# Performance work log

Measured on AMD Instinct MI355X. Metric: run time of the kernel, lower is better.

The kernel has to match this reference:

```python
import jax, jax.numpy as jnp
import numpy as np

N = 30000      # nodes
E = 1000000    # edges
G = 256        # graphs
IN = 3         # in_channels
H = 8          # heads
D = 16         # per-head dim
HID = 128      # hidden_dim = H*D
L = 3          # num_layers
KP = 17        # num_keypoints
KPE = 16       # kp_emb_dim
NEG = 0.2      # GATv2 leaky_relu negative slope
EPS = 1e-5     # BatchNorm eps


def setup_inputs() -> dict:
    key = jax.random.key(0)
    ks = jax.random.split(key, 24)
    x = jax.random.normal(ks[0], (N, IN), jnp.float32)
    edge_index = jax.random.randint(ks[1], (2, E), 0, N, jnp.int32)
    batch = jnp.sort(jax.random.randint(ks[2], (N,), 0, G, jnp.int32))
    s_in = 1.0 / np.sqrt(IN + KPE)
    s_h = 1.0 / np.sqrt(HID)
    return {
        "x": x,
        "edge_index": edge_index,
        "batch": batch,
        "kp_emb": jax.random.normal(ks[3], (KP, KPE), jnp.float32),
        "w_in": jax.random.normal(ks[4], (IN + KPE, HID), jnp.float32) * s_in,
        "b_in": jax.random.normal(ks[5], (HID,), jnp.float32) * 0.01,
        "w_l": jax.random.normal(ks[6], (L, HID, HID), jnp.float32) * s_h,
        "w_r": jax.random.normal(ks[7], (L, HID, HID), jnp.float32) * s_h,
        "att": jax.random.normal(ks[8], (L, H, D), jnp.float32) * (1.0 / np.sqrt(D)),
        "conv_bias": jax.random.normal(ks[9], (L, HID), jnp.float32) * 0.01,
        "bn_gamma": jnp.ones((L, HID), jnp.float32) + 0.1 * jax.random.normal(ks[10], (L, HID), jnp.float32),
        "bn_beta": 0.1 * jax.random.normal(ks[11], (L, HID), jnp.float32),
        "bn_mean": 0.1 * jax.random.normal(ks[12], (L, HID), jnp.float32),
        "bn_var": 0.5 + jax.random.uniform(ks[13], (L, HID), jnp.float32),
        "w1": jax.random.normal(ks[14], (HID, 2 * HID), jnp.float32) * s_h,
        "b1": jnp.zeros((2 * HID,), jnp.float32),
        "w2": jax.random.normal(ks[15], (2 * HID, HID), jnp.float32) * (1.0 / np.sqrt(2 * HID)),
        "b2": jnp.zeros((HID,), jnp.float32),
        "w3": jax.random.normal(ks[16], (HID, 2), jnp.float32) * s_h,
        "b3": jnp.zeros((2,), jnp.float32),
    }


def reference(x, edge_index, batch, kp_emb, w_in, b_in, w_l, w_r, att, conv_bias,
              bn_gamma, bn_beta, bn_mean, bn_var, w1, b1, w2, b2, w3, b3):
    n = x.shape[0]
    # keypoint id embedding concat + input projection
    kp_ids = jnp.arange(n) % KP
    h = jnp.concatenate([x, kp_emb[kp_ids]], axis=-1) @ w_in + b_in  # [N, HID]
    # GATv2Conv adds self loops by default
    loops = jnp.arange(n, dtype=edge_index.dtype)
    src = jnp.concatenate([edge_index[0], loops])  # message sources (j)
    dst = jnp.concatenate([edge_index[1], loops])  # message targets (i)
    for l in range(L):
        xl = (h @ w_l[l]).reshape(n, H, D)  # source transform (lin_l)
        xr = (h @ w_r[l]).reshape(n, H, D)  # target transform (lin_r)
        z = xl[src] + xr[dst]                              # [Et, H, D]
        score = jnp.einsum('ehd,hd->eh', jax.nn.leaky_relu(z, NEG), att[l])
        # segment softmax over incoming edges of each dst node
        m = jax.ops.segment_max(score, dst, num_segments=n)
        ex = jnp.exp(score - m[dst])
        denom = jax.ops.segment_sum(ex, dst, num_segments=n)
        alpha = ex / denom[dst]                            # [Et, H]
        msg = xl[src] * alpha[..., None]                   # [Et, H, D]
        out = jax.ops.segment_sum(msg, dst, num_segments=n).reshape(n, HID) + conv_bias[l]
        out = jax.nn.relu(out)
        # BatchNorm1d (eval mode: running stats)
        out = (out - bn_mean[l]) * (bn_gamma[l] / jnp.sqrt(bn_var[l] + EPS)) + bn_beta[l]
        h = h + out  # residual (dropout = identity in eval)
    # global mean pool per graph
    sums = jax.ops.segment_sum(h, batch, num_segments=G)
    cnt = jax.ops.segment_sum(jnp.ones((n, 1), h.dtype), batch, num_segments=G)
    g = sums / jnp.maximum(cnt, 1.0)
    # classifier MLP
    g = jax.nn.elu(g @ w1 + b1)
    g = jax.nn.elu(g @ w2 + b2)
    return g @ w3 + b3  # [G, 2]
```

## Files before the change

kernel.cpp:

```cpp
#include <hip/hip_runtime.h>
#include <hip/hip_bf16.h>

#define N_NODES 30000
#define N_EDGES 1000000
#define N_GRAPHS 256
#define HEADS 8
#define DHEAD 16
#define HIDDEN 128
#define LAYERS 3
#define KPN 17
#define KPE 16
#define NEG_SLOPE 0.2f
#define BN_EPS 1e-5f
#define ET (N_EDGES + N_NODES)
#define NBIN 235
#define BINW 128
#define BINCAP 6144
#define CHUNK 4096

typedef __attribute__((ext_vector_type(8))) short bf16x8;
typedef __attribute__((ext_vector_type(4))) float f32x4;

__device__ __forceinline__ unsigned bf16_rne(float f) {
    unsigned u = __float_as_uint(f);
    return (u + 0x7fffu + ((u >> 16) & 1u)) >> 16;
}

__global__ __launch_bounds__(256) void k_bin(const int* __restrict__ ei,
                                             int* __restrict__ bcnt,
                                             unsigned* __restrict__ bdata) {
    __shared__ int lcnt[NBIN];
    __shared__ int lbase[NBIN];
    int base = blockIdx.x * CHUNK;
    int n = N_EDGES - base; if (n > CHUNK) n = CHUNK;
    for (int i = threadIdx.x; i < NBIN; i += 256) lcnt[i] = 0;
    __syncthreads();
    for (int t = threadIdx.x; t < n; t += 256) {
        int d = ei[N_EDGES + base + t];
        atomicAdd(&lcnt[d >> 7], 1);
    }
    __syncthreads();
    for (int i = threadIdx.x; i < NBIN; i += 256) {
        int c = lcnt[i];
        lbase[i] = c ? atomicAdd(&bcnt[i], c) : 0;
        lcnt[i] = 0;
    }
    __syncthreads();
    for (int t = threadIdx.x; t < n; t += 256) {
        int s = ei[base + t];
        int d = ei[N_EDGES + base + t];
        int b = d >> 7;
        int pos = lbase[b] + atomicAdd(&lcnt[b], 1);
        bdata[(size_t)b * BINCAP + pos] = (unsigned)s | ((unsigned)(d & 127) << 15);
    }
}

__global__ __launch_bounds__(256) void k_aux(const int* __restrict__ bcnt,
                                             const int* __restrict__ batch,
                                             const float* __restrict__ w_l,
                                             const float* __restrict__ w_r,
                                             int* __restrict__ bbase,
                                             int* __restrict__ ptr,
                                             int* __restrict__ gptr,
                                             unsigned short* __restrict__ wT) {
    int t = threadIdx.x;
    if (blockIdx.x == 0) {
        for (int g = t; g <= N_GRAPHS; g += 256) {
            if (g == N_GRAPHS) { gptr[g] = N_NODES; }
            else {
                int lo = 0, hi = N_NODES;
                while (lo < hi) {
                    int mid = (lo + hi) >> 1;
                    if (batch[mid] < g) lo = mid + 1; else hi = mid;
                }
                gptr[g] = lo;
            }
        }
        __shared__ int v[256];
        int c = 0;
        if (t < NBIN) {
            int nodes = N_NODES - t * BINW; if (nodes > BINW) nodes = BINW;
            c = bcnt[t] + nodes;
        }
        v[t] = c;
        __syncthreads();
        for (int off = 1; off < 256; off <<= 1) {
            int x = (t >= off) ? v[t - off] : 0;
            __syncthreads();
            v[t] += x;
            __syncthreads();
        }
        if (t < NBIN) bbase[t] = v[t] - c;
        if (t == 0) ptr[N_NODES] = ET;
    } else {
        int idx = (blockIdx.x - 1) * 256 + t;
        if (idx < LAYERS * 256 * 128) {
            int l = idx / (256 * 128);
            int rem = idx - l * 256 * 128;
            int c = rem >> 7;
            int k = rem & 127;
            float v = (c < 128) ? w_l[(size_t)l * 16384 + k * 128 + c]
                                : w_r[(size_t)l * 16384 + k * 128 + (c - 128)];
            wT[idx] = (unsigned short)bf16_rne(v);
        }
    }
}

__global__ __launch_bounds__(256) void k_place2(const int* __restrict__ bcnt,
                                                const unsigned* __restrict__ bdata,
                                                const int* __restrict__ bbase,
                                                int* __restrict__ ptr,
                                                unsigned short* __restrict__ csr_src) {
    __shared__ int hist[BINW];
    __shared__ int pre[BINW];
    __shared__ int nodestart[BINW];
    __shared__ int lofs[BINW];
    int b = blockIdx.x;
    int tid = threadIdx.x;
    int nNodes = N_NODES - b * BINW; if (nNodes > BINW) nNodes = BINW;
    int n = bcnt[b];
    if (tid < BINW) hist[tid] = (tid < nNodes) ? 1 : 0;
    __syncthreads();
    for (int t = tid; t < n; t += 256)
        atomicAdd(&hist[(bdata[(size_t)b * BINCAP + t] >> 15) & 127], 1);
    __syncthreads();
    if (tid < BINW) pre[tid] = hist[tid];
    __syncthreads();
    for (int off = 1; off < BINW; off <<= 1) {
        int x = (tid >= off && tid < BINW) ? pre[tid - off] : 0;
        __syncthreads();
        if (tid < BINW) pre[tid] += x;
        __syncthreads();
    }
    if (tid < BINW) {
        int ns = bbase[b] + pre[tid] - hist[tid];
        nodestart[tid] = ns;
        if (tid < nNodes) {
            int node = b * BINW + tid;
            ptr[node] = ns;
            csr_src[ns] = (unsigned short)node;
        }
        lofs[tid] = 1;
    }
    __syncthreads();
    for (int t = tid; t < n; t += 256) {
        unsigned e = bdata[(size_t)b * BINCAP + t];
        int dl = (e >> 15) & 127;
        int pos = nodestart[dl] + atomicAdd(&lofs[dl], 1);
        csr_src[pos] = (unsigned short)(e & 0x7fffu);
    }
}

__global__ void k_inproj(const float* __restrict__ x, const float* __restrict__ kp_emb,
                         const float* __restrict__ w_in, const float* __restrict__ b_in,
                         float* __restrict__ h, unsigned short* __restrict__ hb) {
    int t = blockIdx.x * 256 + threadIdx.x;
    if (t >= N_NODES * HIDDEN) return;
    int c = t & 127, i = t >> 7;
    float acc = b_in[c];
    const float* xi = x + i * 3;
    acc += xi[0] * w_in[0 * 128 + c];
    acc += xi[1] * w_in[1 * 128 + c];
    acc += xi[2] * w_in[2 * 128 + c];
    const float* kp = kp_emb + (i % KPN) * KPE;
#pragma unroll
    for (int k = 0; k < KPE; ++k) acc += kp[k] * w_in[(3 + k) * 128 + c];
    h[t] = acc;
    hb[t] = (unsigned short)bf16_rne(acc);
}

__global__ __launch_bounds__(256) void k_gemm(const unsigned short* __restrict__ hb,
                                              const unsigned short* __restrict__ wT,
                                              unsigned short* __restrict__ xlb,
                                              unsigned short* __restrict__ xrb) {
    int wave = threadIdx.x >> 6;
    int lane = threadIdx.x & 63;
    int brow = blockIdx.x * 32;
    int lr = lane & 15;
    int lk = lane >> 4;
    int ar0 = brow + lr;
    int ar1 = brow + 16 + lr;
    int ar0c = ar0 < N_NODES ? ar0 : N_NODES - 1;
    int ar1c = ar1 < N_NODES ? ar1 : N_NODES - 1;
    int c0 = wave * 64 + lr;

    const unsigned short* ha0 = hb + (size_t)ar0c * 128 + lk * 8;
    const unsigned short* ha1 = hb + (size_t)ar1c * 128 + lk * 8;
    const unsigned short* wb  = wT + (size_t)c0 * 128 + lk * 8;

    f32x4 acc[2][4];
#pragma unroll
    for (int m = 0; m < 2; ++m)
#pragma unroll
        for (int n = 0; n < 4; ++n) acc[m][n] = (f32x4){0.f, 0.f, 0.f, 0.f};

#pragma unroll
    for (int ks = 0; ks < 4; ++ks) {
        bf16x8 a0 = *(const bf16x8*)(ha0 + ks * 32);
        bf16x8 a1 = *(const bf16x8*)(ha1 + ks * 32);
#pragma unroll
        for (int nt = 0; nt < 4; ++nt) {
            bf16x8 b = *(const bf16x8*)(wb + nt * 16 * 128 + ks * 32);
            acc[0][nt] = __builtin_amdgcn_mfma_f32_16x16x32_bf16(a0, b, acc[0][nt], 0, 0, 0);
            acc[1][nt] = __builtin_amdgcn_mfma_f32_16x16x32_bf16(a1, b, acc[1][nt], 0, 0, 0);
        }
    }

    int drow0 = brow + lk * 4;
#pragma unroll
    for (int mt = 0; mt < 2; ++mt) {
#pragma unroll
        for (int nt = 0; nt < 4; ++nt) {
            int col = c0 + nt * 16;
#pragma unroll
            for (int j = 0; j < 4; ++j) {
                int grow = drow0 + mt * 16 + j;
                if (grow >= N_NODES) continue;
                unsigned short bv = (unsigned short)bf16_rne(acc[mt][nt][j]);
                if (col < 128) xlb[(size_t)grow * 128 + col] = bv;
                else           xrb[(size_t)grow * 128 + (col - 128)] = bv;
            }
        }
    }
}

__global__ __launch_bounds__(256) void k_gat(const uint4* __restrict__ xlb4,
                                             const uint4* __restrict__ xrb4,
                                             const int* __restrict__ ptr,
                                             const unsigned short* __restrict__ csr_src,
                                             const float* __restrict__ att_l,
                                             const float* __restrict__ bias_l,
                                             const float* __restrict__ gamma_l,
                                             const float* __restrict__ beta_l,
                                             const float* __restrict__ mean_l,
                                             const float* __restrict__ var_l,
                                             float* __restrict__ h,
                                             unsigned short* __restrict__ hb) {
    int wid = (blockIdx.x * 256 + threadIdx.x) >> 6;
    int lane = threadIdx.x & 63;
    if (wid >= N_NODES) return;
    int i = wid;
    int e4 = lane >> 4;
    int l16 = lane & 15;
    int d0 = 8 * l16;

    uint4 xw = xrb4[(size_t)i * 16 + l16];
    float2 xra = make_float2(__uint_as_float(xw.x << 16), __uint_as_float(xw.x & 0xffff0000u));
    float2 xrb_ = make_float2(__uint_as_float(xw.y << 16), __uint_as_float(xw.y & 0xffff0000u));
    float2 xrc = make_float2(__uint_as_float(xw.z << 16), __uint_as_float(xw.z & 0xffff0000u));
    float2 xrd = make_float2(__uint_as_float(xw.w << 16), __uint_as_float(xw.w & 0xffff0000u));
    const float L2E = 1.44269504089f;
    float4 avA = *(const float4*)(att_l + d0);
    float4 avB = *(const float4*)(att_l + d0 + 4);
    float2 a6a = make_float2(avA.x * (0.6f * L2E), avA.y * (0.6f * L2E));
    float2 a6b = make_float2(avA.z * (0.6f * L2E), avA.w * (0.6f * L2E));
    float2 a6c = make_float2(avB.x * (0.6f * L2E), avB.y * (0.6f * L2E));
    float2 a6d = make_float2(avB.z * (0.6f * L2E), avB.w * (0.6f * L2E));
    float2 a4a = make_float2(avA.x * (0.4f * L2E), avA.y * (0.4f * L2E));
    float2 a4b = make_float2(avA.z * (0.4f * L2E), avA.w * (0.4f * L2E));
    float2 a4c = make_float2(avB.x * (0.4f * L2E), avB.y * (0.4f * L2E));
    float2 a4d = make_float2(avB.z * (0.4f * L2E), avB.w * (0.4f * L2E));
    int e0 = ptr[i], e1 = ptr[i + 1];

    float denom = 0.f;
    float2 acA = make_float2(0.f, 0.f), acB = make_float2(0.f, 0.f);
    float2 acC = make_float2(0.f, 0.f), acD = make_float2(0.f, 0.f);

#define LDQ(KQ, WREG, VREG) { \
    int eo = 4 * (KQ) + e4; \
    int sr = __shfl(sv, eo); \
    VREG = eo < cnt; \
    int rw = VREG ? sr : 0; \
    WREG = xlb4[(size_t)rw * 16 + l16]; \
}
#define PROCQ(WREG, VREG) { \
    float2 va = make_float2(__uint_as_float(WREG.x << 16), __uint_as_float(WREG.x & 0xffff0000u)); \
    float2 vb = make_float2(__uint_as_float(WREG.y << 16), __uint_as_float(WREG.y & 0xffff0000u)); \
    float2 vc = make_float2(__uint_as_float(WREG.z << 16), __uint_as_float(WREG.z & 0xffff0000u)); \
    float2 vd = make_float2(__uint_as_float(WREG.w << 16), __uint_as_float(WREG.w & 0xffff0000u)); \
    float2 za, zb, zc, zd; \
    za.x = va.x + xra.x;  za.y = va.y + xra.y; \
    zb.x = vb.x + xrb_.x; zb.y = vb.y + xrb_.y; \
    zc.x = vc.x + xrc.x;  zc.y = vc.y + xrc.y; \
    zd.x = vd.x + xrd.x;  zd.y = vd.y + xrd.y; \
    float2 p6, p4; \
    p6.x = za.x * a6a.x;  p6.y = za.y * a6a.y; \
    p6.x = fmaf(zb.x, a6b.x, p6.x); p6.y = fmaf(zb.y, a6b.y, p6.y); \
    p6.x = fmaf(zc.x, a6c.x, p6.x); p6.y = fmaf(zc.y, a6c.y, p6.y); \
    p6.x = fmaf(zd.x, a6d.x, p6.x); p6.y = fmaf(zd.y, a6d.y, p6.y); \
    p4.x = fabsf(za.x) * a4a.x;  p4.y = fabsf(za.y) * a4a.y; \
    p4.x = fmaf(fabsf(zb.x), a4b.x, p4.x); p4.y = fmaf(fabsf(zb.y), a4b.y, p4.y); \
    p4.x = fmaf(fabsf(zc.x), a4c.x, p4.x); p4.y = fmaf(fabsf(zc.y), a4c.y, p4.y); \
    p4.x = fmaf(fabsf(zd.x), a4d.x, p4.x); p4.y = fmaf(fabsf(zd.y), a4d.y, p4.y); \
    float p = (p6.x + p4.x) + (p6.y + p4.y); \
    p += __shfl_xor(p, 1); \
    float ex = VREG ? exp2f(p) : 0.f; \
    denom += ex; \
    acA.x = fmaf(ex, va.x, acA.x); acA.y = fmaf(ex, va.y, acA.y); \
    acB.x = fmaf(ex, vb.x, acB.x); acB.y = fmaf(ex, vb.y, acB.y); \
    acC.x = fmaf(ex, vc.x, acC.x); acC.y = fmaf(ex, vc.y, acC.y); \
    acD.x = fmaf(ex, vd.x, acD.x); acD.y = fmaf(ex, vd.y, acD.y); \
}

    for (int base = e0; base < e1; base += 64) {
        int idx = base + lane;
        int sv = (idx < e1) ? (int)csr_src[idx] : 0;
        int cnt = e1 - base; if (cnt > 64) cnt = 64;
        int nq = (cnt + 3) >> 2;

        uint4 w0, w1; bool b0 = false, b1 = false;
        LDQ(0, w0, b0);
        if (1 < nq) LDQ(1, w1, b1);
        int k = 0;
        for (; k + 2 < nq; k += 2) {
            uint4 n0, n1; bool c0v, c1v;
            LDQ(k + 2, n0, c0v);
            LDQ(k + 3, n1, c1v);
            PROCQ(w0, b0); PROCQ(w1, b1);
            w0 = n0; b0 = c0v; w1 = n1; b1 = c1v;
        }
        PROCQ(w0, b0);
        if (k + 1 < nq) PROCQ(w1, b1);
    }
#undef LDQ
#undef PROCQ

    denom += __shfl_xor(denom, 16); denom += __shfl_xor(denom, 32);
    acA.x += __shfl_xor(acA.x, 16); acA.x += __shfl_xor(acA.x, 32);
    acA.y += __shfl_xor(acA.y, 16); acA.y += __shfl_xor(acA.y, 32);
    acB.x += __shfl_xor(acB.x, 16); acB.x += __shfl_xor(acB.x, 32);
    acB.y += __shfl_xor(acB.y, 16); acB.y += __shfl_xor(acB.y, 32);
    acC.x += __shfl_xor(acC.x, 16); acC.x += __shfl_xor(acC.x, 32);
    acC.y += __shfl_xor(acC.y, 16); acC.y += __shfl_xor(acC.y, 32);
    acD.x += __shfl_xor(acD.x, 16); acD.x += __shfl_xor(acD.x, 32);
    acD.y += __shfl_xor(acD.y, 16); acD.y += __shfl_xor(acD.y, 32);

    if (e4 == 0) {
        float inv = 1.f / denom;
        float4 biaA = *(const float4*)(bias_l + d0),  biaB = *(const float4*)(bias_l + d0 + 4);
        float4 gamA = *(const float4*)(gamma_l + d0), gamB = *(const float4*)(gamma_l + d0 + 4);
        float4 betA = *(const float4*)(beta_l + d0),  betB = *(const float4*)(beta_l + d0 + 4);
        float4 meaA = *(const float4*)(mean_l + d0),  meaB = *(const float4*)(mean_l + d0 + 4);
        float4 varA = *(const float4*)(var_l + d0),   varB = *(const float4*)(var_l + d0 + 4);
        float o0 = fmaxf(acA.x * inv + biaA.x, 0.f);
        float o1 = fmaxf(acA.y * inv + biaA.y, 0.f);
        float o2 = fmaxf(acB.x * inv + biaA.z, 0.f);
        float o3 = fmaxf(acB.y * inv + biaA.w, 0.f);
        float o4 = fmaxf(acC.x * inv + biaB.x, 0.f);
        float o5 = fmaxf(acC.y * inv + biaB.y, 0.f);
        float o6 = fmaxf(acD.x * inv + biaB.z, 0.f);
        float o7 = fmaxf(acD.y * inv + biaB.w, 0.f);
        o0 = (o0 - meaA.x) * (gamA.x * rsqrtf(varA.x + BN_EPS)) + betA.x;
        o1 = (o1 - meaA.y) * (gamA.y * rsqrtf(varA.y + BN_EPS)) + betA.y;
        o2 = (o2 - meaA.z) * (gamA.z * rsqrtf(varA.z + BN_EPS)) + betA.z;
        o3 = (o3 - meaA.w) * (gamA.w * rsqrtf(varA.w + BN_EPS)) + betA.w;
        o4 = (o4 - meaB.x) * (gamB.x * rsqrtf(varB.x + BN_EPS)) + betB.x;
        o5 = (o5 - meaB.y) * (gamB.y * rsqrtf(varB.y + BN_EPS)) + betB.y;
        o6 = (o6 - meaB.z) * (gamB.z * rsqrtf(varB.z + BN_EPS)) + betB.z;
        o7 = (o7 - meaB.w) * (gamB.w * rsqrtf(varB.w + BN_EPS)) + betB.w;
        float4 hvA = *(const float4*)(h + (size_t)i * 128 + d0);
        float4 hvB = *(const float4*)(h + (size_t)i * 128 + d0 + 4);
        hvA.x += o0; hvA.y += o1; hvA.z += o2; hvA.w += o3;
        hvB.x += o4; hvB.y += o5; hvB.z += o6; hvB.w += o7;
        *(float4*)(h + (size_t)i * 128 + d0) = hvA;
        *(float4*)(h + (size_t)i * 128 + d0 + 4) = hvB;
        uint4 pk;
        pk.x = bf16_rne(hvA.x) | (bf16_rne(hvA.y) << 16);
        pk.y = bf16_rne(hvA.z) | (bf16_rne(hvA.w) << 16);
        pk.z = bf16_rne(hvB.x) | (bf16_rne(hvB.y) << 16);
        pk.w = bf16_rne(hvB.z) | (bf16_rne(hvB.w) << 16);
        *(uint4*)(hb + (size_t)i * 128 + d0) = pk;
    }
}

__global__ __launch_bounds__(256) void k_poolmlp(const float* __restrict__ h,
                                                 const int* __restrict__ gptr,
                                                 const float* __restrict__ w1, const float* __restrict__ b1,
                                                 const float* __restrict__ w2, const float* __restrict__ b2,
                                                 const float* __restrict__ w3, const float* __restrict__ b3,
                                                 float* __restrict__ out) {
    __shared__ float red[256];
    __shared__ float g[128], t1[256], t2[128];
    int b = blockIdx.x, t = threadIdx.x;
    int c = t & 127, half = t >> 7;
    int lo = gptr[b], hi = gptr[b + 1];
    float s = 0.f;
    for (int i = lo + half; i < hi; i += 2) s += h[(size_t)i * 128 + c];
    red[t] = s;
    __syncthreads();
    if (half == 0) {
        float cntf = fmaxf((float)(hi - lo), 1.0f);
        g[c] = (red[c] + red[c + 128]) / cntf;
    }
    __syncthreads();
    {
        float acc = b1[t];
        for (int k = 0; k < 128; ++k) acc += g[k] * w1[k * 256 + t];
        t1[t] = acc > 0.f ? acc : expm1f(acc);
    }
    __syncthreads();
    if (t < 128) {
        float acc = b2[t];
        for (int k = 0; k < 256; ++k) acc += t1[k] * w2[k * 128 + t];
        t2[t] = acc > 0.f ? acc : expm1f(acc);
    }
    __syncthreads();
    if (t < 2) {
        float acc = b3[t];
        for (int k = 0; k < 128; ++k) acc += t2[k] * w3[k * 2 + t];
        out[b * 2 + t] = acc;
    }
}

extern "C" void kernel_launch(void* const* d_in, const int* in_sizes, int n_in,
                              void* d_out, int out_size, void* d_ws, size_t ws_size,
                              hipStream_t stream) {
    const float* x        = (const float*)d_in[0];
    const int*   ei       = (const int*)d_in[1];
    const int*   batch    = (const int*)d_in[2];
    const float* kp_emb   = (const float*)d_in[3];
    const float* w_in     = (const float*)d_in[4];
    const float* b_in     = (const float*)d_in[5];
    const float* w_l      = (const float*)d_in[6];
    const float* w_r      = (const float*)d_in[7];
    const float* att      = (const float*)d_in[8];
    const float* conv_b   = (const float*)d_in[9];
    const float* bn_gamma = (const float*)d_in[10];
    const float* bn_beta  = (const float*)d_in[11];
    const float* bn_mean  = (const float*)d_in[12];
    const float* bn_var   = (const float*)d_in[13];
    const float* w1 = (const float*)d_in[14];
    const float* b1 = (const float*)d_in[15];
    const float* w2 = (const float*)d_in[16];
    const float* b2 = (const float*)d_in[17];
    const float* w3 = (const float*)d_in[18];
    const float* b3 = (const float*)d_in[19];
    float* out = (float*)d_out;

    char* ws = (char*)d_ws;
    const size_t OFF_H    = 0;
    const size_t OFF_HB   = OFF_H    + 15360000;
    const size_t OFF_XL   = OFF_HB   + 7680000;
    const size_t OFF_XR   = OFF_XL   + 7680000;
    const size_t OFF_WT   = OFF_XR   + 7680000;
    const size_t OFF_PTR  = OFF_WT   + 196608;
    const size_t OFF_BCNT = OFF_PTR  + 120320;
    const size_t OFF_BBAS = OFF_BCNT + 1024;
    const size_t OFF_SRC  = OFF_BBAS + 1024;
    const size_t OFF_GPTR = OFF_SRC  + 2060032;

    float*          h      = (float*)(ws + OFF_H);
    unsigned short* hb     = (unsigned short*)(ws + OFF_HB);
    unsigned short* xlb    = (unsigned short*)(ws + OFF_XL);
    unsigned short* xrb    = (unsigned short*)(ws + OFF_XR);
    unsigned*       bdata  = (unsigned*)(ws + OFF_XR);
    unsigned short* wT     = (unsigned short*)(ws + OFF_WT);
    int*            ptr    = (int*)(ws + OFF_PTR);
    int*            bcnt   = (int*)(ws + OFF_BCNT);
    int*            bbase  = (int*)(ws + OFF_BBAS);
    unsigned short* csrsrc = (unsigned short*)(ws + OFF_SRC);
    int*            gptr   = (int*)(ws + OFF_GPTR);

    hipMemsetAsync(bcnt, 0, NBIN * 4, stream);
    k_bin<<<(N_EDGES + CHUNK - 1) / CHUNK, 256, 0, stream>>>(ei, bcnt, bdata);
    k_aux<<<1 + (LAYERS * 256 * 128 + 255) / 256, 256, 0, stream>>>(bcnt, batch, w_l, w_r,
                                                                    bbase, ptr, gptr, wT);
    k_place2<<<NBIN, 256, 0, stream>>>(bcnt, bdata, bbase, ptr, csrsrc);

    k_inproj<<<(N_NODES * 128 + 255) / 256, 256, 0, stream>>>(x, kp_emb, w_in, b_in, h, hb);

    for (int l = 0; l < LAYERS; ++l) {
        k_gemm<<<(N_NODES + 31) / 32, 256, 0, stream>>>(hb, wT + (size_t)l * 256 * 128, xlb, xrb);
        k_gat<<<(N_NODES + 3) / 4, 256, 0, stream>>>(
            (const uint4*)xlb, (const uint4*)xrb, ptr, csrsrc,
            att + (size_t)l * 128, conv_b + (size_t)l * 128,
            bn_gamma + (size_t)l * 128, bn_beta + (size_t)l * 128,
            bn_mean + (size_t)l * 128, bn_var + (size_t)l * 128, h, hb);
    }

    k_poolmlp<<<N_GRAPHS, 256, 0, stream>>>(h, gptr, w1, b1, w2, b2, w3, b3, out);
}
```

Before: 280.3 us.

## Fuse preprocessing kernels, fold input projection into first GEMM, stage GEMM stores

```diff
diff --git a/kernel.cpp b/kernel.cpp
--- a/kernel.cpp
+++ b/kernel.cpp
@@ -17,6 +17,8 @@
 #define BINW 128
 #define BINCAP 6144
 #define CHUNK 4096
+#define NB_EDGE 245
+#define NB_WCONV 384
 
 typedef __attribute__((ext_vector_type(8))) short bf16x8;
 typedef __attribute__((ext_vector_type(4))) float f32x4;
@@ -28,44 +30,40 @@
 
 __global__ __launch_bounds__(256) void k_bin(const int* __restrict__ ei,
                                              int* __restrict__ bcnt,
-                                             unsigned* __restrict__ bdata) {
-    __shared__ int lcnt[NBIN];
-    __shared__ int lbase[NBIN];
-    int base = blockIdx.x * CHUNK;
-    int n = N_EDGES - base; if (n > CHUNK) n = CHUNK;
-    for (int i = threadIdx.x; i < NBIN; i += 256) lcnt[i] = 0;
-    __syncthreads();
-    for (int t = threadIdx.x; t < n; t += 256) {
-        int d = ei[N_EDGES + base + t];
-        atomicAdd(&lcnt[d >> 7], 1);
-    }
-    __syncthreads();
-    for (int i = threadIdx.x; i < NBIN; i += 256) {
-        int c = lcnt[i];
-        lbase[i] = c ? atomicAdd(&bcnt[i], c) : 0;
-        lcnt[i] = 0;
-    }
-    __syncthreads();
-    for (int t = threadIdx.x; t < n; t += 256) {
-        int s = ei[base + t];
-        int d = ei[N_EDGES + base + t];
-        int b = d >> 7;
-        int pos = lbase[b] + atomicAdd(&lcnt[b], 1);
-        bdata[(size_t)b * BINCAP + pos] = (unsigned)s | ((unsigned)(d & 127) << 15);
-    }
-}
-
-__global__ __launch_bounds__(256) void k_aux(const int* __restrict__ bcnt,
+                                             unsigned* __restrict__ bdata,
                                              const int* __restrict__ batch,
+                                             int* __restrict__ gptr,
                                              const float* __restrict__ w_l,
                                              const float* __restrict__ w_r,
-                                             int* __restrict__ bbase,
-                                             int* __restrict__ ptr,
-                                             int* __restrict__ gptr,
                                              unsigned short* __restrict__ wT) {
-    int t = threadIdx.x;
-    if (blockIdx.x == 0) {
-        for (int g = t; g <= N_GRAPHS; g += 256) {
+    int bid = blockIdx.x;
+    if (bid < NB_EDGE) {
+        __shared__ int lcnt[NBIN];
+        __shared__ int lbase[NBIN];
+        int base = bid * CHUNK;
+        int n = N_EDGES - base; if (n > CHUNK) n = CHUNK;
+        for (int i = threadIdx.x; i < NBIN; i += 256) lcnt[i] = 0;
+        __syncthreads();
+        for (int t = threadIdx.x; t < n; t += 256) {
+            int d = ei[N_EDGES + base + t];
+            atomicAdd(&lcnt[d >> 7], 1);
+        }
+        __syncthreads();
+        for (int i = threadIdx.x; i < NBIN; i += 256) {
+            int c = lcnt[i];
+            lbase[i] = c ? atomicAdd(&bcnt[i], c) : 0;
+            lcnt[i] = 0;
+        }
+        __syncthreads();
+        for (int t = threadIdx.x; t < n; t += 256) {
+            int s = ei[base + t];
+            int d = ei[N_EDGES + base + t];
+            int b = d >> 7;
+            int pos = lbase[b] + atomicAdd(&lcnt[b], 1);
+            bdata[(size_t)b * BINCAP + pos] = (unsigned)s | ((unsigned)(d & 127) << 15);
+        }
+    } else if (bid == NB_EDGE) {
+        for (int g = threadIdx.x; g <= N_GRAPHS; g += 256) {
             if (g == N_GRAPHS) { gptr[g] = N_NODES; }
             else {
                 int lo = 0, hi = N_NODES;
@@ -76,24 +74,8 @@
                 gptr[g] = lo;
             }
         }
-        __shared__ int v[256];
-        int c = 0;
-        if (t < NBIN) {
-            int nodes = N_NODES - t * BINW; if (nodes > BINW) nodes = BINW;
-            c = bcnt[t] + nodes;
-        }
-        v[t] = c;
-        __syncthreads();
-        for (int off = 1; off < 256; off <<= 1) {
-            int x = (t >= off) ? v[t - off] : 0;
-            __syncthreads();
-            v[t] += x;
-            __syncthreads();
-        }
-        if (t < NBIN) bbase[t] = v[t] - c;
-        if (t == 0) ptr[N_NODES] = ET;
     } else {
-        int idx = (blockIdx.x - 1) * 256 + t;
+        int idx = (bid - NB_EDGE - 1) * 256 + threadIdx.x;
         if (idx < LAYERS * 256 * 128) {
             int l = idx / (256 * 128);
             int rem = idx - l * 256 * 128;
@@ -104,6 +86,28 @@
             wT[idx] = (unsigned short)bf16_rne(v);
         }
     }
+}
+
+__global__ __launch_bounds__(256) void k_bscan(const int* __restrict__ bcnt,
+                                               int* __restrict__ bbase,
+                                               int* __restrict__ ptr) {
+    __shared__ int v[256];
+    int t = threadIdx.x;
+    int c = 0;
+    if (t < NBIN) {
+        int nodes = N_NODES - t * BINW; if (nodes > BINW) nodes = BINW;
+        c = bcnt[t] + nodes;
+    }
+    v[t] = c;
+    __syncthreads();
+    for (int off = 1; off < 256; off <<= 1) {
+        int x = (t >= off) ? v[t - off] : 0;
+        __syncthreads();
+        v[t] += x;
+        __syncthreads();
+    }
+    if (t < NBIN) bbase[t] = v[t] - c;
+    if (t == 0) ptr[N_NODES] = ET;
 }
 
 __global__ __launch_bounds__(256) void k_place2(const int* __restrict__ bcnt,
@@ -151,42 +155,53 @@
     }
 }
 
-__global__ void k_inproj(const float* __restrict__ x, const float* __restrict__ kp_emb,
-                         const float* __restrict__ w_in, const float* __restrict__ b_in,
-                         float* __restrict__ h, unsigned short* __restrict__ hb) {
-    int t = blockIdx.x * 256 + threadIdx.x;
-    if (t >= N_NODES * HIDDEN) return;
-    int c = t & 127, i = t >> 7;
-    float acc = b_in[c];
-    const float* xi = x + i * 3;
-    acc += xi[0] * w_in[0 * 128 + c];
-    acc += xi[1] * w_in[1 * 128 + c];
-    acc += xi[2] * w_in[2 * 128 + c];
-    const float* kp = kp_emb + (i % KPN) * KPE;
-#pragma unroll
-    for (int k = 0; k < KPE; ++k) acc += kp[k] * w_in[(3 + k) * 128 + c];
-    h[t] = acc;
-    hb[t] = (unsigned short)bf16_rne(acc);
-}
-
-__global__ __launch_bounds__(256) void k_gemm(const unsigned short* __restrict__ hb,
-                                              const unsigned short* __restrict__ wT,
-                                              unsigned short* __restrict__ xlb,
-                                              unsigned short* __restrict__ xrb) {
-    int wave = threadIdx.x >> 6;
-    int lane = threadIdx.x & 63;
+template<bool FUSED>
+__global__ __launch_bounds__(256) void k_gemmT(const float* __restrict__ x,
+                                               const float* __restrict__ kp_emb,
+                                               const float* __restrict__ w_in,
+                                               const float* __restrict__ b_in,
+                                               float* __restrict__ h,
+                                               const unsigned short* __restrict__ hb,
+                                               const unsigned short* __restrict__ wT,
+                                               unsigned short* __restrict__ xlb,
+                                               unsigned short* __restrict__ xrb) {
+    __shared__ unsigned short hsA[32][136];
+    __shared__ unsigned short st[32][264];
+    int tid = threadIdx.x;
+    int wave = tid >> 6, lane = tid & 63;
     int brow = blockIdx.x * 32;
-    int lr = lane & 15;
-    int lk = lane >> 4;
-    int ar0 = brow + lr;
-    int ar1 = brow + 16 + lr;
-    int ar0c = ar0 < N_NODES ? ar0 : N_NODES - 1;
-    int ar1c = ar1 < N_NODES ? ar1 : N_NODES - 1;
+    int lr = lane & 15, lk = lane >> 4;
+
+    if (FUSED) {
+        int r = tid >> 3, c16 = (tid & 7) * 16;
+        int gr = brow + r;
+        int gc = gr < N_NODES ? gr : 0;
+        float xv0 = x[gc * 3], xv1 = x[gc * 3 + 1], xv2 = x[gc * 3 + 2];
+        const float* kp = kp_emb + (gc % KPN) * KPE;
+        float res[16];
+#pragma unroll
+        for (int q = 0; q < 16; ++q) {
+            int c = c16 + q;
+            float acc = b_in[c] + xv0 * w_in[c] + xv1 * w_in[128 + c] + xv2 * w_in[256 + c];
+#pragma unroll
+            for (int kk = 0; kk < KPE; ++kk) acc += kp[kk] * w_in[(3 + kk) * 128 + c];
+            res[q] = acc;
+        }
+        if (gr < N_NODES) {
+#pragma unroll
+            for (int q = 0; q < 16; q += 4)
+                *(float4*)(h + (size_t)gr * 128 + c16 + q) =
+                    make_float4(res[q], res[q + 1], res[q + 2], res[q + 3]);
+        }
+#pragma unroll
+        for (int q = 0; q < 16; ++q) hsA[r][c16 + q] = (unsigned short)bf16_rne(res[q]);
+        __syncthreads();
+    }
+
+    int ar0c = brow + lr;      if (ar0c >= N_NODES) ar0c = N_NODES - 1;
+    int ar1c = brow + 16 + lr; if (ar1c >= N_NODES) ar1c = N_NODES - 1;
     int c0 = wave * 64 + lr;
-
-    const unsigned short* ha0 = hb + (size_t)ar0c * 128 + lk * 8;
-    const unsigned short* ha1 = hb + (size_t)ar1c * 128 + lk * 8;
-    const unsigned short* wb  = wT + (size_t)c0 * 128 + lk * 8;
+    const unsigned short* wb = wT + (size_t)c0 * 128 + lk * 8;
 
     f32x4 acc[2][4];
 #pragma unroll
@@ -196,8 +211,14 @@
 
 #pragma unroll
     for (int ks = 0; ks < 4; ++ks) {
-        bf16x8 a0 = *(const bf16x8*)(ha0 + ks * 32);
-        bf16x8 a1 = *(const bf16x8*)(ha1 + ks * 32);
+        bf16x8 a0, a1;
+        if (FUSED) {
+            a0 = *(const bf16x8*)&hsA[lr][lk * 8 + ks * 32];
+            a1 = *(const bf16x8*)&hsA[16 + lr][lk * 8 + ks * 32];
+        } else {
+            a0 = *(const bf16x8*)(hb + (size_t)ar0c * 128 + lk * 8 + ks * 32);
+            a1 = *(const bf16x8*)(hb + (size_t)ar1c * 128 + lk * 8 + ks * 32);
+        }
 #pragma unroll
         for (int nt = 0; nt < 4; ++nt) {
             bf16x8 b = *(const bf16x8*)(wb + nt * 16 * 128 + ks * 32);
@@ -206,21 +227,29 @@
         }
     }
 
-    int drow0 = brow + lk * 4;
-#pragma unroll
-    for (int mt = 0; mt < 2; ++mt) {
-#pragma unroll
-        for (int nt = 0; nt < 4; ++nt) {
-            int col = c0 + nt * 16;
-#pragma unroll
-            for (int j = 0; j < 4; ++j) {
-                int grow = drow0 + mt * 16 + j;
-                if (grow >= N_NODES) continue;
-                unsigned short bv = (unsigned short)bf16_rne(acc[mt][nt][j]);
-                if (col < 128) xlb[(size_t)grow * 128 + col] = bv;
-                else           xrb[(size_t)grow * 128 + (col - 128)] = bv;
-            }
-        }
+    int r0 = lk * 4;
+#pragma unroll
+    for (int mt = 0; mt < 2; ++mt)
+#pragma unroll
+        for (int nt = 0; nt < 4; ++nt)
+#pragma unroll
+            for (int j = 0; j < 4; ++j)
+                st[r0 + mt * 16 + j][c0 + nt * 16] = (unsigned short)bf16_rne(acc[mt][nt][j]);
+    __syncthreads();
+
+    int rr = tid >> 3, seg = tid & 7;
+    int grow = brow + rr;
+    if (grow < N_NODES) {
+        uint4 v0 = *(uint4*)&st[rr][seg * 32];
+        uint4 v1 = *(uint4*)&st[rr][seg * 32 + 8];
+        uint4 v2 = *(uint4*)&st[rr][seg * 32 + 16];
+        uint4 v3 = *(uint4*)&st[rr][seg * 32 + 24];
+        unsigned short* dst = (seg < 4) ? (xlb + (size_t)grow * 128 + seg * 32)
+                                        : (xrb + (size_t)grow * 128 + (seg - 4) * 32);
+        *(uint4*)(dst)      = v0;
+        *(uint4*)(dst + 8)  = v1;
+        *(uint4*)(dst + 16) = v2;
+        *(uint4*)(dst + 24) = v3;
     }
 }
 
@@ -308,19 +337,22 @@
         int cnt = e1 - base; if (cnt > 64) cnt = 64;
         int nq = (cnt + 3) >> 2;
 
-        uint4 w0, w1; bool b0 = false, b1 = false;
+        uint4 w0, w1, w2; bool b0 = false, b1 = false, b2 = false;
         LDQ(0, w0, b0);
         if (1 < nq) LDQ(1, w1, b1);
+        if (2 < nq) LDQ(2, w2, b2);
         int k = 0;
-        for (; k + 2 < nq; k += 2) {
-            uint4 n0, n1; bool c0v, c1v;
-            LDQ(k + 2, n0, c0v);
-            LDQ(k + 3, n1, c1v);
-            PROCQ(w0, b0); PROCQ(w1, b1);
-            w0 = n0; b0 = c0v; w1 = n1; b1 = c1v;
+        for (; k + 3 < nq; k += 3) {
+            uint4 n0, n1, n2; bool c0v, c1v, c2v;
+            LDQ(k + 3, n0, c0v);
+            LDQ(k + 4, n1, c1v);
+            LDQ(k + 5, n2, c2v);
+            PROCQ(w0, b0); PROCQ(w1, b1); PROCQ(w2, b2);
+            w0 = n0; b0 = c0v; w1 = n1; b1 = c1v; w2 = n2; b2 = c2v;
         }
         PROCQ(w0, b0);
         if (k + 1 < nq) PROCQ(w1, b1);
+        if (k + 2 < nq) PROCQ(w2, b2);
     }
 #undef LDQ
 #undef PROCQ
@@ -462,15 +494,18 @@
     int*            gptr   = (int*)(ws + OFF_GPTR);
 
     hipMemsetAsync(bcnt, 0, NBIN * 4, stream);
-    k_bin<<<(N_EDGES + CHUNK - 1) / CHUNK, 256, 0, stream>>>(ei, bcnt, bdata);
-    k_aux<<<1 + (LAYERS * 256 * 128 + 255) / 256, 256, 0, stream>>>(bcnt, batch, w_l, w_r,
-                                                                    bbase, ptr, gptr, wT);
+    k_bin<<<NB_EDGE + 1 + NB_WCONV, 256, 0, stream>>>(ei, bcnt, bdata, batch, gptr, w_l, w_r, wT);
+    k_bscan<<<1, 256, 0, stream>>>(bcnt, bbase, ptr);
     k_place2<<<NBIN, 256, 0, stream>>>(bcnt, bdata, bbase, ptr, csrsrc);
 
-    k_inproj<<<(N_NODES * 128 + 255) / 256, 256, 0, stream>>>(x, kp_emb, w_in, b_in, h, hb);
-
     for (int l = 0; l < LAYERS; ++l) {
-        k_gemm<<<(N_NODES + 31) / 32, 256, 0, stream>>>(hb, wT + (size_t)l * 256 * 128, xlb, xrb);
+        const unsigned short* wTl = wT + (size_t)l * 256 * 128;
+        if (l == 0)
+            k_gemmT<true><<<(N_NODES + 31) / 32, 256, 0, stream>>>(
+                x, kp_emb, w_in, b_in, h, hb, wTl, xlb, xrb);
+        else
+            k_gemmT<false><<<(N_NODES + 31) / 32, 256, 0, stream>>>(
+                x, kp_emb, w_in, b_in, h, hb, wTl, xlb, xrb);
         k_gat<<<(N_NODES + 3) / 4, 256, 0, stream>>>(
             (const uint4*)xlb, (const uint4*)xrb, ptr, csrsrc,
             att + (size_t)l * 128, conv_b + (size_t)l * 128,
```

Measured after the change: 286.4 us. 1.02x slower.
